# Performance work log

Hardware: AMD Instinct MI355X
Metric: run time of the kernel (lower is better)

The kernel has to match this reference:

```python
import jax, jax.numpy as jnp
import numpy as np

N_NODES = 50000
N_EDGES = 800000
F_IN = 64
HID = 64
N_CLASSES = 10


def setup_inputs() -> dict:
    key = jax.random.key(0)
    ks = jax.random.split(key, 16)
    features = jax.random.normal(ks[0], (N_NODES, F_IN), dtype=jnp.float32)
    edge_indicies = jax.random.randint(ks[1], (2, N_EDGES), 0, N_NODES, dtype=jnp.int64)
    s = 1.0 / np.sqrt(HID)
    params = {}
    # three GINConv MLPs: Linear(in,64) -> ReLU -> Linear(64,64)
    for i in range(3):
        d_in = F_IN if i == 0 else HID
        si = 1.0 / np.sqrt(d_in)
        params[f"W1_{i}"] = jax.random.uniform(ks[2 + 4 * i], (d_in, HID), jnp.float32, -si, si)
        params[f"b1_{i}"] = jax.random.uniform(ks[3 + 4 * i], (HID,), jnp.float32, -si, si)
        params[f"W2_{i}"] = jax.random.uniform(ks[4 + 4 * i], (HID, HID), jnp.float32, -s, s)
        params[f"b2_{i}"] = jax.random.uniform(ks[5 + 4 * i], (HID,), jnp.float32, -s, s)
    params["W_lin"] = jax.random.uniform(ks[14], (HID, N_CLASSES), jnp.float32, -s, s)
    params["b_lin"] = jax.random.uniform(ks[15], (N_CLASSES,), jnp.float32, -s, s)
    return {"features": features, "edge_indicies": edge_indicies, **params}


def _gin_conv(x, src, dst, W1, b1, W2, b2):
    # aggregate: sum_{j in N(i)} x_j  (messages flow src -> dst), eps = 0
    agg = jax.ops.segment_sum(x[src], dst, num_segments=N_NODES)
    h = agg + x  # (1 + eps) * x + aggregate, eps=0
    # MLP: Linear -> ReLU -> Linear
    return jax.nn.relu(h @ W1 + b1) @ W2 + b2


def reference(features, edge_indicies,
              W1_0, b1_0, W2_0, b2_0,
              W1_1, b1_1, W2_1, b2_1,
              W1_2, b1_2, W2_2, b2_2,
              W_lin, b_lin):
    src, dst = edge_indicies[0], edge_indicies[1]
    x = jax.nn.relu(_gin_conv(features, src, dst, W1_0, b1_0, W2_0, b2_0))
    x = jax.nn.relu(_gin_conv(x, src, dst, W1_1, b1_1, W2_1, b2_1))
    x = jax.nn.relu(_gin_conv(x, src, dst, W1_2, b1_2, W2_2, b2_2))
    return x @ W_lin + b_lin
```

## Files before the change

### kernel.cpp

```cpp
#include <hip/hip_runtime.h>
#include <hip/hip_bf16.h>

#define FDIM 64
#define BNODES 64
#define CHUNK 4096
#define HP 72
#define GCAP 2048
#define SGT 512

typedef short bf16x8 __attribute__((ext_vector_type(8)));
typedef float f32x4 __attribute__((ext_vector_type(4)));

__device__ __forceinline__ unsigned short f2bf(float f) {
    unsigned int u = __float_as_uint(f);
    unsigned int r = (u + 0x7fffu + ((u >> 16) & 1u)) >> 16;
    return (unsigned short)r;
}
__device__ __forceinline__ float bflo(unsigned int p) { return __uint_as_float(p << 16); }
__device__ __forceinline__ float bfhi(unsigned int p) { return __uint_as_float(p & 0xffff0000u); }

__global__ __launch_bounds__(256) void cast_prep_hist(const float* __restrict__ x,
                                                      unsigned short* __restrict__ xb, int n4,
                                                      int ncast,
                                                      const float* __restrict__ W10,
                                                      const float* __restrict__ W20,
                                                      const float* __restrict__ W11,
                                                      const float* __restrict__ W21,
                                                      const float* __restrict__ W12,
                                                      const float* __restrict__ W22,
                                                      unsigned short* __restrict__ wt,
                                                      const int* __restrict__ dst,
                                                      int* __restrict__ hist,
                                                      int n_edges, int nbuck) {
    int tid = threadIdx.x;
    if (blockIdx.x < (unsigned)ncast) {
        int i = blockIdx.x * 256 + tid;
        if (i < n4) {
            float4 v = ((const float4*)x)[i];
            uint2 o;
            o.x = (unsigned int)f2bf(v.x) | ((unsigned int)f2bf(v.y) << 16);
            o.y = (unsigned int)f2bf(v.z) | ((unsigned int)f2bf(v.w) << 16);
            ((uint2*)xb)[i] = o;
        }
        return;
    }
    if (blockIdx.x < (unsigned)(ncast + 6)) {
        __shared__ unsigned short s[64 * 64];
        int wsel = blockIdx.x - ncast;
        const float* W;
        switch (wsel) {
            case 0: W = W10; break;
            case 1: W = W20; break;
            case 2: W = W11; break;
            case 3: W = W21; break;
            case 4: W = W12; break;
            default: W = W22; break;
        }
#pragma unroll
        for (int p = 0; p < 4; p++) {
            int idx = tid + p * 256;
            int k = idx >> 4;
            int n0 = (idx & 15) * 4;
            float4 v = ((const float4*)W)[idx];
            s[(n0 + 0) * 64 + k] = f2bf(v.x);
            s[(n0 + 1) * 64 + k] = f2bf(v.y);
            s[(n0 + 2) * 64 + k] = f2bf(v.z);
            s[(n0 + 3) * 64 + k] = f2bf(v.w);
        }
        __syncthreads();
        uint4* o = (uint4*)(wt + (size_t)wsel * 4096);
#pragma unroll
        for (int p = 0; p < 2; p++) {
            int idx = tid + p * 256;
            o[idx] = ((uint4*)s)[idx];
        }
        return;
    }
    {
        __shared__ int lh[1024];
        int chunk = blockIdx.x - ncast - 6;
        for (int i = tid; i < nbuck; i += 256) lh[i] = 0;
        __syncthreads();
        int beg = chunk * CHUNK;
        int end = min(beg + CHUNK, n_edges);
        for (int e = beg + tid; e < end; e += 256)
            atomicAdd(&lh[dst[e] >> 6], 1);
        __syncthreads();
        for (int i = tid; i < nbuck; i += 256)
            hist[(size_t)chunk * nbuck + i] = lh[i];
    }
}

__global__ __launch_bounds__(256) void scan_chunks(const int* __restrict__ hist,
                                                   int* __restrict__ chunk_off,
                                                   int* __restrict__ bucket_total,
                                                   int nchunks, int nbuck) {
    __shared__ int s[256];
    int b = blockIdx.x;
    int t = threadIdx.x;
    int v = (t < nchunks) ? hist[(size_t)t * nbuck + b] : 0;
    s[t] = v;
    __syncthreads();
    for (int off = 1; off < 256; off <<= 1) {
        int u = (t >= off) ? s[t - off] : 0;
        __syncthreads();
        s[t] += u;
        __syncthreads();
    }
    if (t < nchunks) chunk_off[(size_t)t * nbuck + b] = s[t] - v;
    if (t == 255) bucket_total[b] = s[255];
}

__global__ __launch_bounds__(1024) void scan_buckets(const int* __restrict__ bucket_total,
                                                     int* __restrict__ bucket_start,
                                                     int* __restrict__ row_ptr,
                                                     int nbuck, int n_nodes, int n_edges) {
    __shared__ int s[1024];
    int t = threadIdx.x;
    int v = (t < nbuck) ? bucket_total[t] : 0;
    s[t] = v;
    __syncthreads();
    for (int off = 1; off < 1024; off <<= 1) {
        int u = (t >= off) ? s[t - off] : 0;
        __syncthreads();
        s[t] += u;
        __syncthreads();
    }
    if (t < nbuck) bucket_start[t] = s[t] - v;
    if (t == 0) { bucket_start[nbuck] = n_edges; row_ptr[n_nodes] = n_edges; }
}

__global__ __launch_bounds__(256) void bucket_fill(const int* __restrict__ src,
                                                   const int* __restrict__ dst,
                                                   const int* __restrict__ bucket_start,
                                                   const int* __restrict__ chunk_off,
                                                   unsigned int* __restrict__ packed,
                                                   int n_edges, int nbuck) {
    __shared__ int cur[1024];
    int chunk = blockIdx.x;
    for (int i = threadIdx.x; i < nbuck; i += 256)
        cur[i] = bucket_start[i] + chunk_off[(size_t)chunk * nbuck + i];
    __syncthreads();
    int beg = chunk * CHUNK;
    int end = min(beg + CHUNK, n_edges);
    for (int e = beg + threadIdx.x; e < end; e += 256) {
        int d = dst[e];
        int b = d >> 6;
        int pos = atomicAdd(&cur[b], 1);
        packed[pos] = (unsigned int)src[e] | ((unsigned int)(d & 63) << 16);
    }
}

__global__ __launch_bounds__(SGT) void sort_gather(const unsigned int* __restrict__ packed,
                                                   const int* __restrict__ bucket_start,
                                                   const unsigned short* __restrict__ xb,
                                                   int* __restrict__ src_sorted,
                                                   int* __restrict__ row_ptr,
                                                   unsigned short* __restrict__ hb,
                                                   int n_nodes) {
    __shared__ unsigned int spk[GCAP];
    __shared__ int sidx[GCAP];
    __shared__ int cnt[BNODES];
    __shared__ int nbeg[BNODES];
    __shared__ int cur[BNODES];
    int b = blockIdx.x;
    int tid = threadIdx.x;
    int ebeg = bucket_start[b], eend = bucket_start[b + 1];
    int total = eend - ebeg;
    bool fits = (total <= GCAP);
    if (tid < BNODES) cnt[tid] = 0;
    if (fits)
        for (int i = tid; i < total; i += SGT) spk[i] = packed[ebeg + i];
    __syncthreads();
    if (fits) {
        for (int i = tid; i < total; i += SGT) atomicAdd(&cnt[spk[i] >> 16], 1);
    } else {
        for (int e = ebeg + tid; e < eend; e += SGT) atomicAdd(&cnt[packed[e] >> 16], 1);
    }
    __syncthreads();
    if (tid < 64) {
        int v = cnt[tid];
        int inc = v;
#pragma unroll
        for (int off = 1; off < 64; off <<= 1) {
            int u = __shfl_up(inc, off, 64);
            if (tid >= off) inc += u;
        }
        int ex = inc - v;
        nbeg[tid] = ex;
        cur[tid] = ex;
        int node = b * BNODES + tid;
        if (node < n_nodes) row_ptr[node] = ebeg + ex;
    }
    __syncthreads();
    if (fits) {
        for (int i = tid; i < total; i += SGT) {
            unsigned int p = spk[i];
            int pos = atomicAdd(&cur[p >> 16], 1);
            int s = (int)(p & 0xFFFFu);
            sidx[pos] = s;
            src_sorted[ebeg + pos] = s;
        }
    } else {
        for (int e = ebeg + tid; e < eend; e += SGT) {
            unsigned int p = packed[e];
            int pos = atomicAdd(&cur[p >> 16], 1);
            src_sorted[ebeg + pos] = (int)(p & 0xFFFFu);
        }
    }
    __syncthreads();

    int nl = tid >> 3;
    int node = b * BNODES + nl;
    if (node >= n_nodes) return;
    int c = (tid & 7) * 8;
    int dbeg = nbeg[nl];
    int dend = dbeg + cnt[nl];

    float acc[8];
    {
        uint4 v = *(const uint4*)(xb + (size_t)node * FDIM + c);
        acc[0] = bflo(v.x); acc[1] = bfhi(v.x);
        acc[2] = bflo(v.y); acc[3] = bfhi(v.y);
        acc[4] = bflo(v.z); acc[5] = bfhi(v.z);
        acc[6] = bflo(v.w); acc[7] = bfhi(v.w);
    }

    if (fits) {
        int e = dbeg;
        for (; e + 7 < dend; e += 8) {
            int s[8];
#pragma unroll
            for (int j = 0; j < 8; j++) s[j] = sidx[e + j];
            uint4 v[8];
#pragma unroll
            for (int j = 0; j < 8; j++) v[j] = *(const uint4*)(xb + (size_t)s[j] * FDIM + c);
#pragma unroll
            for (int j = 0; j < 8; j++) {
                acc[0] += bflo(v[j].x); acc[1] += bfhi(v[j].x);
                acc[2] += bflo(v[j].y); acc[3] += bfhi(v[j].y);
                acc[4] += bflo(v[j].z); acc[5] += bfhi(v[j].z);
                acc[6] += bflo(v[j].w); acc[7] += bfhi(v[j].w);
            }
        }
        if (e + 3 < dend) {
            int s[4];
#pragma unroll
            for (int j = 0; j < 4; j++) s[j] = sidx[e + j];
            uint4 v[4];
#pragma unroll
            for (int j = 0; j < 4; j++) v[j] = *(const uint4*)(xb + (size_t)s[j] * FDIM + c);
#pragma unroll
            for (int j = 0; j < 4; j++) {
                acc[0] += bflo(v[j].x); acc[1] += bfhi(v[j].x);
                acc[2] += bflo(v[j].y); acc[3] += bfhi(v[j].y);
                acc[4] += bflo(v[j].z); acc[5] += bfhi(v[j].z);
                acc[6] += bflo(v[j].w); acc[7] += bfhi(v[j].w);
            }
            e += 4;
        }
        for (; e < dend; e++) {
            uint4 v = *(const uint4*)(xb + (size_t)sidx[e] * FDIM + c);
            acc[0] += bflo(v.x); acc[1] += bfhi(v.x);
            acc[2] += bflo(v.y); acc[3] += bfhi(v.y);
            acc[4] += bflo(v.z); acc[5] += bfhi(v.z);
            acc[6] += bflo(v.w); acc[7] += bfhi(v.w);
        }
    } else {
        for (int e = dbeg; e < dend; e++) {
            uint4 v = *(const uint4*)(xb + (size_t)src_sorted[ebeg + e] * FDIM + c);
            acc[0] += bflo(v.x); acc[1] += bfhi(v.x);
            acc[2] += bflo(v.y); acc[3] += bfhi(v.y);
            acc[4] += bflo(v.z); acc[5] += bfhi(v.z);
            acc[6] += bflo(v.w); acc[7] += bfhi(v.w);
        }
    }

    uint4 p;
    p.x = (unsigned int)f2bf(acc[0]) | ((unsigned int)f2bf(acc[1]) << 16);
    p.y = (unsigned int)f2bf(acc[2]) | ((unsigned int)f2bf(acc[3]) << 16);
    p.z = (unsigned int)f2bf(acc[4]) | ((unsigned int)f2bf(acc[5]) << 16);
    p.w = (unsigned int)f2bf(acc[6]) | ((unsigned int)f2bf(acc[7]) << 16);
    *(uint4*)(hb + (size_t)node * FDIM + c) = p;
}

__global__ __launch_bounds__(256) void gather_bf16(const unsigned short* __restrict__ xb,
                                                   const int* __restrict__ row_ptr,
                                                   const int* __restrict__ src_sorted,
                                                   unsigned short* __restrict__ hb,
                                                   int n_nodes) {
    __shared__ int sidx[GCAP];
    int base = blockIdx.x * 32;
    int ebeg = row_ptr[base];
    int eend = row_ptr[min(base + 32, n_nodes)];
    int total = eend - ebeg;
    int cnt = min(total, GCAP);
    for (int i = threadIdx.x; i < cnt; i += 256) sidx[i] = src_sorted[ebeg + i];
    __syncthreads();

    int t = threadIdx.x;
    int node = base + (t >> 3);
    if (node >= n_nodes) return;
    int c = (t & 7) * 8;
    int dbeg = row_ptr[node] - ebeg;
    int dend = row_ptr[node + 1] - ebeg;
    int dmid = (total <= GCAP) ? dend : min(dend, cnt);

    float acc[8];
    {
        uint4 v = *(const uint4*)(xb + (size_t)node * FDIM + c);
        acc[0] = bflo(v.x); acc[1] = bfhi(v.x);
        acc[2] = bflo(v.y); acc[3] = bfhi(v.y);
        acc[4] = bflo(v.z); acc[5] = bfhi(v.z);
        acc[6] = bflo(v.w); acc[7] = bfhi(v.w);
    }

    int e = dbeg;
    for (; e + 7 < dmid; e += 8) {
        int s[8];
#pragma unroll
        for (int j = 0; j < 8; j++) s[j] = sidx[e + j];
        uint4 v[8];
#pragma unroll
        for (int j = 0; j < 8; j++) v[j] = *(const uint4*)(xb + (size_t)s[j] * FDIM + c);
#pragma unroll
        for (int j = 0; j < 8; j++) {
            acc[0] += bflo(v[j].x); acc[1] += bfhi(v[j].x);
            acc[2] += bflo(v[j].y); acc[3] += bfhi(v[j].y);
            acc[4] += bflo(v[j].z); acc[5] += bfhi(v[j].z);
            acc[6] += bflo(v[j].w); acc[7] += bfhi(v[j].w);
        }
    }
    if (e + 3 < dmid) {
        int s[4];
#pragma unroll
        for (int j = 0; j < 4; j++) s[j] = sidx[e + j];
        uint4 v[4];
#pragma unroll
        for (int j = 0; j < 4; j++) v[j] = *(const uint4*)(xb + (size_t)s[j] * FDIM + c);
#pragma unroll
        for (int j = 0; j < 4; j++) {
            acc[0] += bflo(v[j].x); acc[1] += bfhi(v[j].x);
            acc[2] += bflo(v[j].y); acc[3] += bfhi(v[j].y);
            acc[4] += bflo(v[j].z); acc[5] += bfhi(v[j].z);
            acc[6] += bflo(v[j].w); acc[7] += bfhi(v[j].w);
        }
        e += 4;
    }
    for (; e < dmid; e++) {
        uint4 v = *(const uint4*)(xb + (size_t)sidx[e] * FDIM + c);
        acc[0] += bflo(v.x); acc[1] += bfhi(v.x);
        acc[2] += bflo(v.y); acc[3] += bfhi(v.y);
        acc[4] += bflo(v.z); acc[5] += bfhi(v.z);
        acc[6] += bflo(v.w); acc[7] += bfhi(v.w);
    }
    for (; e < dend; e++) {
        uint4 v = *(const uint4*)(xb + (size_t)src_sorted[ebeg + e] * FDIM + c);
        acc[0] += bflo(v.x); acc[1] += bfhi(v.x);
        acc[2] += bflo(v.y); acc[3] += bfhi(v.y);
        acc[4] += bflo(v.z); acc[5] += bfhi(v.z);
        acc[6] += bflo(v.w); acc[7] += bfhi(v.w);
    }

    uint4 p;
    p.x = (unsigned int)f2bf(acc[0]) | ((unsigned int)f2bf(acc[1]) << 16);
    p.y = (unsigned int)f2bf(acc[2]) | ((unsigned int)f2bf(acc[3]) << 16);
    p.z = (unsigned int)f2bf(acc[4]) | ((unsigned int)f2bf(acc[5]) << 16);
    p.w = (unsigned int)f2bf(acc[6]) | ((unsigned int)f2bf(acc[7]) << 16);
    *(uint4*)(hb + (size_t)node * FDIM + c) = p;
}

__global__ __launch_bounds__(256) void mlp_mfma(const unsigned short* __restrict__ xb,
        const unsigned short* __restrict__ wt1, const float* __restrict__ b1,
        const unsigned short* __restrict__ wt2, const float* __restrict__ b2,
        const float* __restrict__ Wl, const float* __restrict__ bl,
        unsigned short* __restrict__ y, float* __restrict__ out,
        int n_nodes, int do_final) {
    __shared__ unsigned short sH[64 * HP];
    __shared__ unsigned short sW1t[64 * HP];
    __shared__ unsigned short sW2t[64 * HP];
    __shared__ float sb1[FDIM], sb2[FDIM];
    __shared__ float sWl[FDIM * 10];
    __shared__ float sbl[16];

    int tid = threadIdx.x;
    int base = blockIdx.x * 64;

    {
        const uint4* w1g = (const uint4*)wt1;
        const uint4* w2g = (const uint4*)wt2;
#pragma unroll
        for (int p = 0; p < 2; p++) {
            int idx = tid + p * 256;
            int r = idx >> 3, q = idx & 7;
            *(uint4*)(&sW1t[r * HP + q * 8]) = w1g[idx];
            *(uint4*)(&sW2t[r * HP + q * 8]) = w2g[idx];
        }
    }
    if (tid < FDIM) { sb1[tid] = b1[tid]; sb2[tid] = b2[tid]; }
    if (do_final) {
        for (int i = tid; i < FDIM * 10; i += 256) sWl[i] = Wl[i];
        if (tid < 10) sbl[tid] = bl[tid];
    }
#pragma unroll
    for (int p = 0; p < 2; p++) {
        int idx = tid + p * 256;
        int r = idx >> 3, q = idx & 7;
        uint4 v = make_uint4(0u, 0u, 0u, 0u);
        if (base + r < n_nodes) v = *(const uint4*)(xb + (size_t)(base + r) * FDIM + q * 8);
        *(uint4*)(&sH[r * HP + q * 8]) = v;
    }
    __syncthreads();

    int w = tid >> 6;
    int lane = tid & 63;
    int qd = lane >> 4;
    int m = lane & 15;
    int arow = (w * 16 + m) * HP;

    f32x4 acc[4];

    {
        bf16x8 a0 = *(bf16x8*)(&sH[arow + qd * 8]);
        bf16x8 a1 = *(bf16x8*)(&sH[arow + 32 + qd * 8]);
#pragma unroll
        for (int t = 0; t < 4; t++) {
            float bias = sb1[t * 16 + m];
            acc[t] = (f32x4){bias, bias, bias, bias};
            bf16x8 bA = *(bf16x8*)(&sW1t[(t * 16 + m) * HP + qd * 8]);
            bf16x8 bB = *(bf16x8*)(&sW1t[(t * 16 + m) * HP + 32 + qd * 8]);
            acc[t] = __builtin_amdgcn_mfma_f32_16x16x32_bf16(a0, bA, acc[t], 0, 0, 0);
            acc[t] = __builtin_amdgcn_mfma_f32_16x16x32_bf16(a1, bB, acc[t], 0, 0, 0);
        }
#pragma unroll
        for (int t = 0; t < 4; t++)
#pragma unroll
            for (int r = 0; r < 4; r++)
                sH[(w * 16 + qd * 4 + r) * HP + t * 16 + m] = f2bf(fmaxf(acc[t][r], 0.f));
    }

    {
        bf16x8 a0 = *(bf16x8*)(&sH[arow + qd * 8]);
        bf16x8 a1 = *(bf16x8*)(&sH[arow + 32 + qd * 8]);
#pragma unroll
        for (int t = 0; t < 4; t++) {
            float bias = sb2[t * 16 + m];
            acc[t] = (f32x4){bias, bias, bias, bias};
            bf16x8 bA = *(bf16x8*)(&sW2t[(t * 16 + m) * HP + qd * 8]);
            bf16x8 bB = *(bf16x8*)(&sW2t[(t * 16 + m) * HP + 32 + qd * 8]);
            acc[t] = __builtin_amdgcn_mfma_f32_16x16x32_bf16(a0, bA, acc[t], 0, 0, 0);
            acc[t] = __builtin_amdgcn_mfma_f32_16x16x32_bf16(a1, bB, acc[t], 0, 0, 0);
        }
#pragma unroll
        for (int t = 0; t < 4; t++)
#pragma unroll
            for (int r = 0; r < 4; r++)
                sH[(w * 16 + qd * 4 + r) * HP + t * 16 + m] = f2bf(fmaxf(acc[t][r], 0.f));
    }
    __syncthreads();

    if (!do_final) {
#pragma unroll
        for (int p = 0; p < 2; p++) {
            int idx = tid + p * 256;
            int r = idx >> 3, q = idx & 7;
            if (base + r < n_nodes)
                *(uint4*)(y + (size_t)(base + r) * FDIM + q * 8) = *(uint4*)(&sH[r * HP + q * 8]);
        }
    } else {
        for (int i = tid; i < 64 * 10; i += 256) {
            int nl = i / 10, cc = i % 10;
            int node = base + nl;
            if (node < n_nodes) {
                float s = sbl[cc];
#pragma unroll
                for (int k0 = 0; k0 < FDIM; k0 += 4) {
                    uint2 hp = *(uint2*)(&sH[nl * HP + k0]);
                    s += bflo(hp.x) * sWl[(k0 + 0) * 10 + cc] + bfhi(hp.x) * sWl[(k0 + 1) * 10 + cc]
                       + bflo(hp.y) * sWl[(k0 + 2) * 10 + cc] + bfhi(hp.y) * sWl[(k0 + 3) * 10 + cc];
                }
                out[(size_t)node * 10 + cc] = s;
            }
        }
    }
}

extern "C" void kernel_launch(void* const* d_in, const int* in_sizes, int n_in,
                              void* d_out, int out_size, void* d_ws, size_t ws_size,
                              hipStream_t stream) {
    const float* features = (const float*)d_in[0];
    const int* edges = (const int*)d_in[1];
    int n_nodes = in_sizes[0] / FDIM;
    int n_edges = in_sizes[1] / 2;
    const int* src = edges;
    const int* dst = edges + n_edges;

    int nbuck = (n_nodes + BNODES - 1) / BNODES;
    int nchunks = (n_edges + CHUNK - 1) / CHUNK;

    int* hist = (int*)d_ws;
    int* chunk_off = hist + (size_t)nchunks * nbuck;
    int* bucket_total = chunk_off + (size_t)nchunks * nbuck;
    int* bucket_start = bucket_total + nbuck;
    int* row_ptr = bucket_start + nbuck + 1;
    unsigned int* packed = (unsigned int*)(row_ptr + n_nodes + 1);
    int* src_sorted = (int*)(packed + n_edges);
    size_t int_elems = 2 * (size_t)nchunks * nbuck + 2 * (size_t)nbuck + 2
                       + (size_t)n_nodes + 2 * (size_t)n_edges;
    int_elems = (int_elems + 3) & ~(size_t)3;
    size_t buf_elems = (size_t)n_nodes * FDIM;
    unsigned short* hb  = (unsigned short*)((int*)d_ws + int_elems);
    unsigned short* xb0 = hb + buf_elems;
    unsigned short* yA  = xb0 + buf_elems;
    unsigned short* yB  = yA + buf_elems;
    unsigned short* wt  = yB + buf_elems;

    dim3 bs(256);
    int n4 = (int)(buf_elems / 4);
    int ncast = (n4 + 255) / 256;
    dim3 gs_cph(ncast + 6 + nchunks);
    dim3 gs_gather((n_nodes + 31) / 32);
    dim3 gs_tile((n_nodes + 63) / 64);

    cast_prep_hist<<<gs_cph, bs, 0, stream>>>(features, xb0, n4, ncast,
                                              (const float*)d_in[2], (const float*)d_in[4],
                                              (const float*)d_in[6], (const float*)d_in[8],
                                              (const float*)d_in[10], (const float*)d_in[12], wt,
                                              dst, hist, n_edges, nbuck);

    scan_chunks<<<nbuck, 256, 0, stream>>>(hist, chunk_off, bucket_total, nchunks, nbuck);
    scan_buckets<<<1, 1024, 0, stream>>>(bucket_total, bucket_start, row_ptr, nbuck, n_nodes, n_edges);
    bucket_fill<<<nchunks, 256, 0, stream>>>(src, dst, bucket_start, chunk_off, packed, n_edges, nbuck);

    const float* Wl = (const float*)d_in[14];
    const float* bl = (const float*)d_in[15];

    sort_gather<<<nbuck, SGT, 0, stream>>>(packed, bucket_start, xb0,
                                           src_sorted, row_ptr, hb, n_nodes);
    mlp_mfma<<<gs_tile, bs, 0, stream>>>(hb, wt, (const float*)d_in[3],
                                         wt + 4096, (const float*)d_in[5], Wl, bl,
                                         yA, (float*)d_out, n_nodes, 0);

    const unsigned short* x_cur = yA;
    unsigned short* outs2[2] = {yB, yA};
    for (int conv = 1; conv < 3; conv++) {
        const float* b1 = (const float*)d_in[3 + 4 * conv];
        const float* b2 = (const float*)d_in[5 + 4 * conv];
        const unsigned short* wt1 = wt + (size_t)(2 * conv) * 4096;
        const unsigned short* wt2 = wt + (size_t)(2 * conv + 1) * 4096;
        int fin = (conv == 2) ? 1 : 0;

        gather_bf16<<<gs_gather, bs, 0, stream>>>(x_cur, row_ptr, src_sorted, hb, n_nodes);
        mlp_mfma<<<gs_tile, bs, 0, stream>>>(hb, wt1, b1, wt2, b2, Wl, bl,
                                             outs2[conv - 1], (float*)d_out, n_nodes, fin);
        x_cur = outs2[conv - 1];
    }
}
```

Measured before the change: 192.4 us.

## Fuse neighbor gather with per-tile MLP into a single conv kernel

The separate gather and MLP kernels for each GIN layer become one kernel, conv_fused. It gathers neighbor sums for 64 nodes into shared memory as bf16, then runs the MFMA MLP on that tile in place. This removes the round trip of the aggregated hidden buffer through global memory and three kernel launches. The first layer also absorbs the per-bucket sort. Weights are now read straight from global memory instead of being staged in LDS, and each thread covers 16 features with 4 threads per node instead of 8, which lowers memory-level parallelism in the gather.

```diff
diff --git a/kernel.cpp b/kernel.cpp
--- a/kernel.cpp
+++ b/kernel.cpp
@@ -6,7 +6,6 @@
 #define CHUNK 4096
 #define HP 72
 #define GCAP 2048
-#define SGT 512
 
 typedef short bf16x8 __attribute__((ext_vector_type(8)));
 typedef float f32x4 __attribute__((ext_vector_type(4)));
@@ -151,264 +150,177 @@
     }
 }
 
-__global__ __launch_bounds__(SGT) void sort_gather(const unsigned int* __restrict__ packed,
-                                                   const int* __restrict__ bucket_start,
-                                                   const unsigned short* __restrict__ xb,
-                                                   int* __restrict__ src_sorted,
-                                                   int* __restrict__ row_ptr,
-                                                   unsigned short* __restrict__ hb,
-                                                   int n_nodes) {
-    __shared__ unsigned int spk[GCAP];
-    __shared__ int sidx[GCAP];
-    __shared__ int cnt[BNODES];
-    __shared__ int nbeg[BNODES];
-    __shared__ int cur[BNODES];
-    int b = blockIdx.x;
-    int tid = threadIdx.x;
-    int ebeg = bucket_start[b], eend = bucket_start[b + 1];
-    int total = eend - ebeg;
-    bool fits = (total <= GCAP);
-    if (tid < BNODES) cnt[tid] = 0;
-    if (fits)
-        for (int i = tid; i < total; i += SGT) spk[i] = packed[ebeg + i];
-    __syncthreads();
-    if (fits) {
-        for (int i = tid; i < total; i += SGT) atomicAdd(&cnt[spk[i] >> 16], 1);
-    } else {
-        for (int e = ebeg + tid; e < eend; e += SGT) atomicAdd(&cnt[packed[e] >> 16], 1);
-    }
-    __syncthreads();
-    if (tid < 64) {
-        int v = cnt[tid];
-        int inc = v;
-#pragma unroll
-        for (int off = 1; off < 64; off <<= 1) {
-            int u = __shfl_up(inc, off, 64);
-            if (tid >= off) inc += u;
-        }
-        int ex = inc - v;
-        nbeg[tid] = ex;
-        cur[tid] = ex;
-        int node = b * BNODES + tid;
-        if (node < n_nodes) row_ptr[node] = ebeg + ex;
-    }
-    __syncthreads();
-    if (fits) {
-        for (int i = tid; i < total; i += SGT) {
-            unsigned int p = spk[i];
-            int pos = atomicAdd(&cur[p >> 16], 1);
-            int s = (int)(p & 0xFFFFu);
-            sidx[pos] = s;
-            src_sorted[ebeg + pos] = s;
-        }
-    } else {
-        for (int e = ebeg + tid; e < eend; e += SGT) {
-            unsigned int p = packed[e];
-            int pos = atomicAdd(&cur[p >> 16], 1);
-            src_sorted[ebeg + pos] = (int)(p & 0xFFFFu);
-        }
-    }
-    __syncthreads();
-
-    int nl = tid >> 3;
-    int node = b * BNODES + nl;
-    if (node >= n_nodes) return;
-    int c = (tid & 7) * 8;
-    int dbeg = nbeg[nl];
-    int dend = dbeg + cnt[nl];
-
-    float acc[8];
-    {
-        uint4 v = *(const uint4*)(xb + (size_t)node * FDIM + c);
-        acc[0] = bflo(v.x); acc[1] = bfhi(v.x);
-        acc[2] = bflo(v.y); acc[3] = bfhi(v.y);
-        acc[4] = bflo(v.z); acc[5] = bfhi(v.z);
-        acc[6] = bflo(v.w); acc[7] = bfhi(v.w);
-    }
-
-    if (fits) {
-        int e = dbeg;
-        for (; e + 7 < dend; e += 8) {
-            int s[8];
-#pragma unroll
-            for (int j = 0; j < 8; j++) s[j] = sidx[e + j];
-            uint4 v[8];
-#pragma unroll
-            for (int j = 0; j < 8; j++) v[j] = *(const uint4*)(xb + (size_t)s[j] * FDIM + c);
-#pragma unroll
-            for (int j = 0; j < 8; j++) {
-                acc[0] += bflo(v[j].x); acc[1] += bfhi(v[j].x);
-                acc[2] += bflo(v[j].y); acc[3] += bfhi(v[j].y);
-                acc[4] += bflo(v[j].z); acc[5] += bfhi(v[j].z);
-                acc[6] += bflo(v[j].w); acc[7] += bfhi(v[j].w);
-            }
-        }
-        if (e + 3 < dend) {
-            int s[4];
-#pragma unroll
-            for (int j = 0; j < 4; j++) s[j] = sidx[e + j];
-            uint4 v[4];
-#pragma unroll
-            for (int j = 0; j < 4; j++) v[j] = *(const uint4*)(xb + (size_t)s[j] * FDIM + c);
-#pragma unroll
-            for (int j = 0; j < 4; j++) {
-                acc[0] += bflo(v[j].x); acc[1] += bfhi(v[j].x);
-                acc[2] += bflo(v[j].y); acc[3] += bfhi(v[j].y);
-                acc[4] += bflo(v[j].z); acc[5] += bfhi(v[j].z);
-                acc[6] += bflo(v[j].w); acc[7] += bfhi(v[j].w);
-            }
-            e += 4;
-        }
-        for (; e < dend; e++) {
-            uint4 v = *(const uint4*)(xb + (size_t)sidx[e] * FDIM + c);
-            acc[0] += bflo(v.x); acc[1] += bfhi(v.x);
-            acc[2] += bflo(v.y); acc[3] += bfhi(v.y);
-            acc[4] += bflo(v.z); acc[5] += bfhi(v.z);
-            acc[6] += bflo(v.w); acc[7] += bfhi(v.w);
-        }
-    } else {
-        for (int e = dbeg; e < dend; e++) {
-            uint4 v = *(const uint4*)(xb + (size_t)src_sorted[ebeg + e] * FDIM + c);
-            acc[0] += bflo(v.x); acc[1] += bfhi(v.x);
-            acc[2] += bflo(v.y); acc[3] += bfhi(v.y);
-            acc[4] += bflo(v.z); acc[5] += bfhi(v.z);
-            acc[6] += bflo(v.w); acc[7] += bfhi(v.w);
-        }
-    }
-
-    uint4 p;
-    p.x = (unsigned int)f2bf(acc[0]) | ((unsigned int)f2bf(acc[1]) << 16);
-    p.y = (unsigned int)f2bf(acc[2]) | ((unsigned int)f2bf(acc[3]) << 16);
-    p.z = (unsigned int)f2bf(acc[4]) | ((unsigned int)f2bf(acc[5]) << 16);
-    p.w = (unsigned int)f2bf(acc[6]) | ((unsigned int)f2bf(acc[7]) << 16);
-    *(uint4*)(hb + (size_t)node * FDIM + c) = p;
-}
-
-__global__ __launch_bounds__(256) void gather_bf16(const unsigned short* __restrict__ xb,
-                                                   const int* __restrict__ row_ptr,
-                                                   const int* __restrict__ src_sorted,
-                                                   unsigned short* __restrict__ hb,
-                                                   int n_nodes) {
-    __shared__ int sidx[GCAP];
-    int base = blockIdx.x * 32;
-    int ebeg = row_ptr[base];
-    int eend = row_ptr[min(base + 32, n_nodes)];
-    int total = eend - ebeg;
-    int cnt = min(total, GCAP);
-    for (int i = threadIdx.x; i < cnt; i += 256) sidx[i] = src_sorted[ebeg + i];
-    __syncthreads();
-
-    int t = threadIdx.x;
-    int node = base + (t >> 3);
-    if (node >= n_nodes) return;
-    int c = (t & 7) * 8;
-    int dbeg = row_ptr[node] - ebeg;
-    int dend = row_ptr[node + 1] - ebeg;
-    int dmid = (total <= GCAP) ? dend : min(dend, cnt);
-
-    float acc[8];
-    {
-        uint4 v = *(const uint4*)(xb + (size_t)node * FDIM + c);
-        acc[0] = bflo(v.x); acc[1] = bfhi(v.x);
-        acc[2] = bflo(v.y); acc[3] = bfhi(v.y);
-        acc[4] = bflo(v.z); acc[5] = bfhi(v.z);
-        acc[6] = bflo(v.w); acc[7] = bfhi(v.w);
-    }
-
-    int e = dbeg;
-    for (; e + 7 < dmid; e += 8) {
-        int s[8];
-#pragma unroll
-        for (int j = 0; j < 8; j++) s[j] = sidx[e + j];
-        uint4 v[8];
-#pragma unroll
-        for (int j = 0; j < 8; j++) v[j] = *(const uint4*)(xb + (size_t)s[j] * FDIM + c);
-#pragma unroll
-        for (int j = 0; j < 8; j++) {
-            acc[0] += bflo(v[j].x); acc[1] += bfhi(v[j].x);
-            acc[2] += bflo(v[j].y); acc[3] += bfhi(v[j].y);
-            acc[4] += bflo(v[j].z); acc[5] += bfhi(v[j].z);
-            acc[6] += bflo(v[j].w); acc[7] += bfhi(v[j].w);
-        }
-    }
-    if (e + 3 < dmid) {
-        int s[4];
-#pragma unroll
-        for (int j = 0; j < 4; j++) s[j] = sidx[e + j];
-        uint4 v[4];
-#pragma unroll
-        for (int j = 0; j < 4; j++) v[j] = *(const uint4*)(xb + (size_t)s[j] * FDIM + c);
-#pragma unroll
-        for (int j = 0; j < 4; j++) {
-            acc[0] += bflo(v[j].x); acc[1] += bfhi(v[j].x);
-            acc[2] += bflo(v[j].y); acc[3] += bfhi(v[j].y);
-            acc[4] += bflo(v[j].z); acc[5] += bfhi(v[j].z);
-            acc[6] += bflo(v[j].w); acc[7] += bfhi(v[j].w);
-        }
-        e += 4;
-    }
-    for (; e < dmid; e++) {
-        uint4 v = *(const uint4*)(xb + (size_t)sidx[e] * FDIM + c);
-        acc[0] += bflo(v.x); acc[1] += bfhi(v.x);
-        acc[2] += bflo(v.y); acc[3] += bfhi(v.y);
-        acc[4] += bflo(v.z); acc[5] += bfhi(v.z);
-        acc[6] += bflo(v.w); acc[7] += bfhi(v.w);
-    }
-    for (; e < dend; e++) {
-        uint4 v = *(const uint4*)(xb + (size_t)src_sorted[ebeg + e] * FDIM + c);
-        acc[0] += bflo(v.x); acc[1] += bfhi(v.x);
-        acc[2] += bflo(v.y); acc[3] += bfhi(v.y);
-        acc[4] += bflo(v.z); acc[5] += bfhi(v.z);
-        acc[6] += bflo(v.w); acc[7] += bfhi(v.w);
-    }
-
-    uint4 p;
-    p.x = (unsigned int)f2bf(acc[0]) | ((unsigned int)f2bf(acc[1]) << 16);
-    p.y = (unsigned int)f2bf(acc[2]) | ((unsigned int)f2bf(acc[3]) << 16);
-    p.z = (unsigned int)f2bf(acc[4]) | ((unsigned int)f2bf(acc[5]) << 16);
-    p.w = (unsigned int)f2bf(acc[6]) | ((unsigned int)f2bf(acc[7]) << 16);
-    *(uint4*)(hb + (size_t)node * FDIM + c) = p;
-}
-
-__global__ __launch_bounds__(256) void mlp_mfma(const unsigned short* __restrict__ xb,
+#define ACCUM(v0, v1)                                          \
+    acc[0] += bflo((v0).x); acc[1] += bfhi((v0).x);            \
+    acc[2] += bflo((v0).y); acc[3] += bfhi((v0).y);            \
+    acc[4] += bflo((v0).z); acc[5] += bfhi((v0).z);            \
+    acc[6] += bflo((v0).w); acc[7] += bfhi((v0).w);            \
+    acc[8] += bflo((v1).x); acc[9] += bfhi((v1).x);            \
+    acc[10] += bflo((v1).y); acc[11] += bfhi((v1).y);          \
+    acc[12] += bflo((v1).z); acc[13] += bfhi((v1).z);          \
+    acc[14] += bflo((v1).w); acc[15] += bfhi((v1).w);
+
+__global__ __launch_bounds__(256) void conv_fused(
+        const unsigned short* __restrict__ xb,
+        const unsigned int* __restrict__ packed,
+        const int* __restrict__ bucket_start,
+        int* __restrict__ src_sorted,
+        int* __restrict__ row_ptr,
         const unsigned short* __restrict__ wt1, const float* __restrict__ b1,
         const unsigned short* __restrict__ wt2, const float* __restrict__ b2,
         const float* __restrict__ Wl, const float* __restrict__ bl,
         unsigned short* __restrict__ y, float* __restrict__ out,
-        int n_nodes, int do_final) {
-    __shared__ unsigned short sH[64 * HP];
-    __shared__ unsigned short sW1t[64 * HP];
-    __shared__ unsigned short sW2t[64 * HP];
-    __shared__ float sb1[FDIM], sb2[FDIM];
+        int n_nodes, int do_sort, int do_final) {
+    __shared__ __align__(16) unsigned char ubuf[16384];
+    unsigned int* spk = (unsigned int*)ubuf;
+    int* sidx = (int*)(ubuf + 8192);
+    unsigned short* sH = (unsigned short*)ubuf;
+    __shared__ int cnt[BNODES], nbeg[BNODES], cur[BNODES];
     __shared__ float sWl[FDIM * 10];
     __shared__ float sbl[16];
 
+    int b = blockIdx.x;
     int tid = threadIdx.x;
-    int base = blockIdx.x * 64;
-
-    {
-        const uint4* w1g = (const uint4*)wt1;
-        const uint4* w2g = (const uint4*)wt2;
-#pragma unroll
-        for (int p = 0; p < 2; p++) {
-            int idx = tid + p * 256;
-            int r = idx >> 3, q = idx & 7;
-            *(uint4*)(&sW1t[r * HP + q * 8]) = w1g[idx];
-            *(uint4*)(&sW2t[r * HP + q * 8]) = w2g[idx];
-        }
-    }
-    if (tid < FDIM) { sb1[tid] = b1[tid]; sb2[tid] = b2[tid]; }
+    int base = b * BNODES;
+
     if (do_final) {
         for (int i = tid; i < FDIM * 10; i += 256) sWl[i] = Wl[i];
         if (tid < 10) sbl[tid] = bl[tid];
     }
-#pragma unroll
-    for (int p = 0; p < 2; p++) {
-        int idx = tid + p * 256;
-        int r = idx >> 3, q = idx & 7;
-        uint4 v = make_uint4(0u, 0u, 0u, 0u);
-        if (base + r < n_nodes) v = *(const uint4*)(xb + (size_t)(base + r) * FDIM + q * 8);
-        *(uint4*)(&sH[r * HP + q * 8]) = v;
+
+    int nl = tid >> 2;
+    int node = base + nl;
+    bool valid = node < n_nodes;
+    int q = (tid & 3) * 16;
+
+    int ebeg, total, dbeg = 0, dcnt = 0;
+    bool fits;
+
+    if (do_sort) {
+        ebeg = bucket_start[b];
+        int eend = bucket_start[b + 1];
+        total = eend - ebeg;
+        fits = (total <= GCAP);
+        if (tid < BNODES) cnt[tid] = 0;
+        if (fits)
+            for (int i = tid; i < total; i += 256) spk[i] = packed[ebeg + i];
+        __syncthreads();
+        if (fits) {
+            for (int i = tid; i < total; i += 256) atomicAdd(&cnt[spk[i] >> 16], 1);
+        } else {
+            for (int e = ebeg + tid; e < eend; e += 256) atomicAdd(&cnt[packed[e] >> 16], 1);
+        }
+        __syncthreads();
+        if (tid < 64) {
+            int v = cnt[tid];
+            int inc = v;
+#pragma unroll
+            for (int off = 1; off < 64; off <<= 1) {
+                int u = __shfl_up(inc, off, 64);
+                if (tid >= off) inc += u;
+            }
+            int ex = inc - v;
+            nbeg[tid] = ex;
+            cur[tid] = ex;
+            int nd = base + tid;
+            if (nd < n_nodes) row_ptr[nd] = ebeg + ex;
+        }
+        __syncthreads();
+        if (fits) {
+            for (int i = tid; i < total; i += 256) {
+                unsigned int p = spk[i];
+                int pos = atomicAdd(&cur[p >> 16], 1);
+                int s = (int)(p & 0xFFFFu);
+                sidx[pos] = s;
+                src_sorted[ebeg + pos] = s;
+            }
+        } else {
+            for (int e = ebeg + tid; e < eend; e += 256) {
+                unsigned int p = packed[e];
+                int pos = atomicAdd(&cur[p >> 16], 1);
+                src_sorted[ebeg + pos] = (int)(p & 0xFFFFu);
+            }
+        }
+        __syncthreads();
+        dbeg = nbeg[nl];
+        dcnt = cnt[nl];
+    } else {
+        ebeg = row_ptr[base];
+        int eend = row_ptr[min(base + BNODES, n_nodes)];
+        total = eend - ebeg;
+        fits = (total <= GCAP);
+        int stage = fits ? total : GCAP;
+        for (int i = tid; i < stage; i += 256) sidx[i] = src_sorted[ebeg + i];
+        int rb = valid ? row_ptr[node] : ebeg;
+        int re = valid ? row_ptr[node + 1] : ebeg;
+        dbeg = rb - ebeg;
+        dcnt = re - rb;
+        __syncthreads();
+    }
+
+    int dend = dbeg + dcnt;
+    int dmid;
+    if (fits) dmid = dend;
+    else if (do_sort) dmid = dbeg;
+    else dmid = min(dend, GCAP);
+
+    float acc[16];
+    if (valid) {
+        const uint4* xr = (const uint4*)(xb + (size_t)node * FDIM + q);
+        uint4 v0 = xr[0], v1 = xr[1];
+        acc[0] = bflo(v0.x); acc[1] = bfhi(v0.x);
+        acc[2] = bflo(v0.y); acc[3] = bfhi(v0.y);
+        acc[4] = bflo(v0.z); acc[5] = bfhi(v0.z);
+        acc[6] = bflo(v0.w); acc[7] = bfhi(v0.w);
+        acc[8] = bflo(v1.x); acc[9] = bfhi(v1.x);
+        acc[10] = bflo(v1.y); acc[11] = bfhi(v1.y);
+        acc[12] = bflo(v1.z); acc[13] = bfhi(v1.z);
+        acc[14] = bflo(v1.w); acc[15] = bfhi(v1.w);
+    } else {
+#pragma unroll
+        for (int i = 0; i < 16; i++) acc[i] = 0.f;
+    }
+
+    int e = dbeg;
+    for (; e + 3 < dmid; e += 4) {
+        int s[4];
+#pragma unroll
+        for (int j = 0; j < 4; j++) s[j] = sidx[e + j];
+        uint4 va[4], vb[4];
+#pragma unroll
+        for (int j = 0; j < 4; j++) {
+            const uint4* p = (const uint4*)(xb + (size_t)s[j] * FDIM + q);
+            va[j] = p[0];
+            vb[j] = p[1];
+        }
+#pragma unroll
+        for (int j = 0; j < 4; j++) { ACCUM(va[j], vb[j]); }
+    }
+    for (; e < dmid; e++) {
+        const uint4* p = (const uint4*)(xb + (size_t)sidx[e] * FDIM + q);
+        uint4 v0 = p[0], v1 = p[1];
+        ACCUM(v0, v1);
+    }
+    for (; e < dend; e++) {
+        const uint4* p = (const uint4*)(xb + (size_t)src_sorted[ebeg + e] * FDIM + q);
+        uint4 v0 = p[0], v1 = p[1];
+        ACCUM(v0, v1);
+    }
+
+    __syncthreads();
+
+    {
+        uint4 p0, p1;
+        p0.x = (unsigned int)f2bf(acc[0]) | ((unsigned int)f2bf(acc[1]) << 16);
+        p0.y = (unsigned int)f2bf(acc[2]) | ((unsigned int)f2bf(acc[3]) << 16);
+        p0.z = (unsigned int)f2bf(acc[4]) | ((unsigned int)f2bf(acc[5]) << 16);
+        p0.w = (unsigned int)f2bf(acc[6]) | ((unsigned int)f2bf(acc[7]) << 16);
+        p1.x = (unsigned int)f2bf(acc[8]) | ((unsigned int)f2bf(acc[9]) << 16);
+        p1.y = (unsigned int)f2bf(acc[10]) | ((unsigned int)f2bf(acc[11]) << 16);
+        p1.z = (unsigned int)f2bf(acc[12]) | ((unsigned int)f2bf(acc[13]) << 16);
+        p1.w = (unsigned int)f2bf(acc[14]) | ((unsigned int)f2bf(acc[15]) << 16);
+        *(uint4*)(&sH[nl * HP + q]) = p0;
+        *(uint4*)(&sH[nl * HP + q + 8]) = p1;
     }
     __syncthreads();
 
@@ -418,25 +330,25 @@
     int m = lane & 15;
     int arow = (w * 16 + m) * HP;
 
-    f32x4 acc[4];
+    f32x4 a4[4];
 
     {
         bf16x8 a0 = *(bf16x8*)(&sH[arow + qd * 8]);
         bf16x8 a1 = *(bf16x8*)(&sH[arow + 32 + qd * 8]);
 #pragma unroll
         for (int t = 0; t < 4; t++) {
-            float bias = sb1[t * 16 + m];
-            acc[t] = (f32x4){bias, bias, bias, bias};
-            bf16x8 bA = *(bf16x8*)(&sW1t[(t * 16 + m) * HP + qd * 8]);
-            bf16x8 bB = *(bf16x8*)(&sW1t[(t * 16 + m) * HP + 32 + qd * 8]);
-            acc[t] = __builtin_amdgcn_mfma_f32_16x16x32_bf16(a0, bA, acc[t], 0, 0, 0);
-            acc[t] = __builtin_amdgcn_mfma_f32_16x16x32_bf16(a1, bB, acc[t], 0, 0, 0);
+            float bias = b1[t * 16 + m];
+            a4[t] = (f32x4){bias, bias, bias, bias};
+            bf16x8 bA = *(const bf16x8*)(wt1 + (size_t)(t * 16 + m) * FDIM + qd * 8);
+            bf16x8 bB = *(const bf16x8*)(wt1 + (size_t)(t * 16 + m) * FDIM + 32 + qd * 8);
+            a4[t] = __builtin_amdgcn_mfma_f32_16x16x32_bf16(a0, bA, a4[t], 0, 0, 0);
+            a4[t] = __builtin_amdgcn_mfma_f32_16x16x32_bf16(a1, bB, a4[t], 0, 0, 0);
         }
 #pragma unroll
         for (int t = 0; t < 4; t++)
 #pragma unroll
             for (int r = 0; r < 4; r++)
-                sH[(w * 16 + qd * 4 + r) * HP + t * 16 + m] = f2bf(fmaxf(acc[t][r], 0.f));
+                sH[(w * 16 + qd * 4 + r) * HP + t * 16 + m] = f2bf(fmaxf(a4[t][r], 0.f));
     }
 
     {
@@ -444,18 +356,18 @@
         bf16x8 a1 = *(bf16x8*)(&sH[arow + 32 + qd * 8]);
 #pragma unroll
         for (int t = 0; t < 4; t++) {
-            float bias = sb2[t * 16 + m];
-            acc[t] = (f32x4){bias, bias, bias, bias};
-            bf16x8 bA = *(bf16x8*)(&sW2t[(t * 16 + m) * HP + qd * 8]);
-            bf16x8 bB = *(bf16x8*)(&sW2t[(t * 16 + m) * HP + 32 + qd * 8]);
-            acc[t] = __builtin_amdgcn_mfma_f32_16x16x32_bf16(a0, bA, acc[t], 0, 0, 0);
-            acc[t] = __builtin_amdgcn_mfma_f32_16x16x32_bf16(a1, bB, acc[t], 0, 0, 0);
+            float bias = b2[t * 16 + m];
+            a4[t] = (f32x4){bias, bias, bias, bias};
+            bf16x8 bA = *(const bf16x8*)(wt2 + (size_t)(t * 16 + m) * FDIM + qd * 8);
+            bf16x8 bB = *(const bf16x8*)(wt2 + (size_t)(t * 16 + m) * FDIM + 32 + qd * 8);
+            a4[t] = __builtin_amdgcn_mfma_f32_16x16x32_bf16(a0, bA, a4[t], 0, 0, 0);
+            a4[t] = __builtin_amdgcn_mfma_f32_16x16x32_bf16(a1, bB, a4[t], 0, 0, 0);
         }
 #pragma unroll
         for (int t = 0; t < 4; t++)
 #pragma unroll
             for (int r = 0; r < 4; r++)
-                sH[(w * 16 + qd * 4 + r) * HP + t * 16 + m] = f2bf(fmaxf(acc[t][r], 0.f));
+                sH[(w * 16 + qd * 4 + r) * HP + t * 16 + m] = f2bf(fmaxf(a4[t][r], 0.f));
     }
     __syncthreads();
 
@@ -463,23 +375,23 @@
 #pragma unroll
         for (int p = 0; p < 2; p++) {
             int idx = tid + p * 256;
-            int r = idx >> 3, q = idx & 7;
+            int r = idx >> 3, qq = idx & 7;
             if (base + r < n_nodes)
-                *(uint4*)(y + (size_t)(base + r) * FDIM + q * 8) = *(uint4*)(&sH[r * HP + q * 8]);
+                *(uint4*)(y + (size_t)(base + r) * FDIM + qq * 8) = *(uint4*)(&sH[r * HP + qq * 8]);
         }
     } else {
         for (int i = tid; i < 64 * 10; i += 256) {
-            int nl = i / 10, cc = i % 10;
-            int node = base + nl;
-            if (node < n_nodes) {
+            int n2 = i / 10, cc = i % 10;
+            int nd = base + n2;
+            if (nd < n_nodes) {
                 float s = sbl[cc];
 #pragma unroll
                 for (int k0 = 0; k0 < FDIM; k0 += 4) {
-                    uint2 hp = *(uint2*)(&sH[nl * HP + k0]);
+                    uint2 hp = *(uint2*)(&sH[n2 * HP + k0]);
                     s += bflo(hp.x) * sWl[(k0 + 0) * 10 + cc] + bfhi(hp.x) * sWl[(k0 + 1) * 10 + cc]
                        + bflo(hp.y) * sWl[(k0 + 2) * 10 + cc] + bfhi(hp.y) * sWl[(k0 + 3) * 10 + cc];
                 }
-                out[(size_t)node * 10 + cc] = s;
+                out[(size_t)nd * 10 + cc] = s;
             }
         }
     }
@@ -514,13 +426,12 @@
     unsigned short* yA  = xb0 + buf_elems;
     unsigned short* yB  = yA + buf_elems;
     unsigned short* wt  = yB + buf_elems;
+    (void)hb;
 
     dim3 bs(256);
     int n4 = (int)(buf_elems / 4);
     int ncast = (n4 + 255) / 256;
     dim3 gs_cph(ncast + 6 + nchunks);
-    dim3 gs_gather((n_nodes + 31) / 32);
-    dim3 gs_tile((n_nodes + 63) / 64);
 
     cast_prep_hist<<<gs_cph, bs, 0, stream>>>(features, xb0, n4, ncast,
                                               (const float*)d_in[2], (const float*)d_in[4],
@@ -535,24 +446,18 @@
     const float* Wl = (const float*)d_in[14];
     const float* bl = (const float*)d_in[15];
 
-    sort_gather<<<nbuck, SGT, 0, stream>>>(packed, bucket_start, xb0,
-                                           src_sorted, row_ptr, hb, n_nodes);
-    mlp_mfma<<<gs_tile, bs, 0, stream>>>(hb, wt, (const float*)d_in[3],
-                                         wt + 4096, (const float*)d_in[5], Wl, bl,
-                                         yA, (float*)d_out, n_nodes, 0);
-
-    const unsigned short* x_cur = yA;
-    unsigned short* outs2[2] = {yB, yA};
-    for (int conv = 1; conv < 3; conv++) {
-        const float* b1 = (const float*)d_in[3 + 4 * conv];
-        const float* b2 = (const float*)d_in[5 + 4 * conv];
-        const unsigned short* wt1 = wt + (size_t)(2 * conv) * 4096;
-        const unsigned short* wt2 = wt + (size_t)(2 * conv + 1) * 4096;
-        int fin = (conv == 2) ? 1 : 0;
-
-        gather_bf16<<<gs_gather, bs, 0, stream>>>(x_cur, row_ptr, src_sorted, hb, n_nodes);
-        mlp_mfma<<<gs_tile, bs, 0, stream>>>(hb, wt1, b1, wt2, b2, Wl, bl,
-                                             outs2[conv - 1], (float*)d_out, n_nodes, fin);
-        x_cur = outs2[conv - 1];
-    }
-}
+    conv_fused<<<nbuck, bs, 0, stream>>>(xb0, packed, bucket_start, src_sorted, row_ptr,
+                                         wt, (const float*)d_in[3],
+                                         wt + 4096, (const float*)d_in[5],
+                                         Wl, bl, yA, (float*)d_out, n_nodes, 1, 0);
+
+    conv_fused<<<nbuck, bs, 0, stream>>>(yA, packed, bucket_start, src_sorted, row_ptr,
+                                         wt + 2 * 4096, (const float*)d_in[7],
+                                         wt + 3 * 4096, (const float*)d_in[9],
+                                         Wl, bl, yB, (float*)d_out, n_nodes, 0, 0);
+
+    conv_fused<<<nbuck, bs, 0, stream>>>(yB, packed, bucket_start, src_sorted, row_ptr,
+                                         wt + 4 * 4096, (const float*)d_in[11],
+                                         wt + 5 * 4096, (const float*)d_in[13],
+                                         Wl, bl, yA, (float*)d_out, n_nodes, 0, 1);
+}
```

After: 193.1 us, median of 2. No clear change (+0.4%).
